# Kernel tuning notes

Measured on AMD Instinct MI355X. Metric: run time of the kernel, lower is better.

The kernel has to match this reference:

```python
import jax, jax.numpy as jnp
import numpy as np

N = 100000
E = 1600000
F_IN, HID, OUT = 64, 64, 32

def setup_inputs() -> dict:
    key = jax.random.key(0)
    ks = jax.random.split(key, 16)
    s = 0.05
    return {
        "x": jax.random.normal(ks[0], (N, F_IN), jnp.float32),
        "edge_index": jax.random.randint(ks[1], (2, E), 0, N, jnp.int64),
        "edge_attr": jax.random.uniform(ks[2], (E, 1), jnp.float32),
        # distance_processor: Linear(1,16) -> ReLU -> Linear(16,1)
        "Wd1": jax.random.normal(ks[3], (1, 16), jnp.float32) * s,
        "bd1": jnp.zeros((16,), jnp.float32),
        "Wd2": jax.random.normal(ks[4], (16, 1), jnp.float32) * s,
        "bd2": jnp.zeros((1,), jnp.float32),
        # conv1 / conv2 GCN linear weights (in, out) + post-aggregation bias
        "W1c": jax.random.normal(ks[5], (F_IN, HID), jnp.float32) * s,
        "b1c": jnp.zeros((HID,), jnp.float32),
        "W2c": jax.random.normal(ks[6], (HID, HID), jnp.float32) * s,
        "b2c": jnp.zeros((HID,), jnp.float32),
        # output head Linear(hidden, output)
        "Wo": jax.random.normal(ks[7], (HID, OUT), jnp.float32) * s,
        "bo": jnp.zeros((OUT,), jnp.float32),
    }


def _gcn_conv(x, src, dst, ew, W, b, n_nodes):
    """PyG GCNConv with edge weights: add self-loops (weight 1), symmetric norm."""
    h = x @ W                                            # [N, out]
    loop = jnp.arange(n_nodes, dtype=src.dtype)
    src_a = jnp.concatenate([src, loop])                 # [E+N]
    dst_a = jnp.concatenate([dst, loop])
    ew_a = jnp.concatenate([ew, jnp.ones((n_nodes,), ew.dtype)])
    deg = jax.ops.segment_sum(ew_a, dst_a, num_segments=n_nodes)
    dinv = jnp.where(deg > 0, jax.lax.rsqrt(jnp.maximum(deg, 1e-30)), 0.0)
    norm = dinv[src_a] * ew_a * dinv[dst_a]              # [E+N]
    msg = norm[:, None] * h[src_a]                       # gather + scale
    agg = jax.ops.segment_sum(msg, dst_a, num_segments=n_nodes)  # scatter-add
    return agg + b


def reference(x, edge_index, edge_attr, Wd1, bd1, Wd2, bd2, W1c, b1c, W2c, b2c, Wo, bo):
    src, dst = edge_index[0], edge_index[1]
    # edge weight from tiny MLP on distance, squeezed to [E]
    hmlp = jax.nn.relu(edge_attr @ Wd1 + bd1)
    ew = jax.nn.sigmoid(hmlp @ Wd2 + bd2)[:, 0]
    h = jax.nn.relu(_gcn_conv(x, src, dst, ew, W1c, b1c, N))
    # dropout is identity in eval mode
    h = _gcn_conv(h, src, dst, ew, W2c, b2c, N)
    return h @ Wo + bo
```

## Files before the change

### kernel.cpp

```cpp
#include <hip/hip_runtime.h>
#include <hip/hip_fp16.h>
#include <math.h>

#define NBMAX 400

__device__ inline ushort f2bf(float f) {
    unsigned u = __float_as_uint(f);
    u += 0x7fff + ((u >> 16) & 1);
    return (ushort)(u >> 16);
}
__device__ inline float bf2f(ushort u) {
    return __uint_as_float(((unsigned)u) << 16);
}

__global__ __launch_bounds__(256) void k_tobf16(const float4* __restrict__ X4,
                                                ushort4* __restrict__ Y4, int n4) {
    int i = blockIdx.x * 256 + threadIdx.x;
    if (i >= n4) return;
    float4 v = X4[i];
    ushort4 o;
    o.x = f2bf(v.x); o.y = f2bf(v.y); o.z = f2bf(v.z); o.w = f2bf(v.w);
    Y4[i] = o;
}

__global__ __launch_bounds__(256) void k_hist(const int* __restrict__ dstv,
                                              int* __restrict__ bcnt,
                                              int E, int chunk) {
    __shared__ int lh[NBMAX];
    int tid = threadIdx.x;
    for (int i = tid; i < NBMAX; i += 256) lh[i] = 0;
    __syncthreads();
    int start = blockIdx.x * chunk;
    int end = min(E, start + chunk);
    for (int e = start + tid; e < end; e += 256)
        atomicAdd(&lh[dstv[e] >> 8], 1);
    __syncthreads();
    for (int i = tid; i < NBMAX; i += 256)
        if (lh[i]) atomicAdd(&bcnt[i], lh[i]);
}

__global__ __launch_bounds__(512) void k_scan_b(const int* __restrict__ bcnt,
                                                int* __restrict__ bbase,
                                                int* __restrict__ bcursor, int nb) {
    __shared__ int s[512];
    int t = threadIdx.x;
    int c = (t < nb) ? bcnt[t] : 0;
    s[t] = c;
    __syncthreads();
    for (int o = 1; o < 512; o <<= 1) {
        int v = (t >= o) ? s[t - o] : 0;
        __syncthreads();
        s[t] += v;
        __syncthreads();
    }
    if (t < nb) {
        int excl = s[t] - c;
        bbase[t] = excl;
        bcursor[t] = excl;
    }
}

__global__ __launch_bounds__(256) void k_edge_scatter(const float* __restrict__ ea,
                                                      const float* __restrict__ Wd1,
                                                      const float* __restrict__ bd1,
                                                      const float* __restrict__ Wd2,
                                                      const float* __restrict__ bd2,
                                                      const int* __restrict__ srcv,
                                                      const int* __restrict__ dstv,
                                                      int* __restrict__ bcursor,
                                                      int2* __restrict__ spk,
                                                      int E, int chunk) {
    __shared__ float w1[16], b1[16], w2[16];
    __shared__ float b2s;
    __shared__ int lh[NBMAX], gb[NBMAX], lc[NBMAX];
    int tid = threadIdx.x;
    if (tid < 16) {
        w1[tid] = Wd1[tid];
        b1[tid] = bd1[tid];
        w2[tid] = Wd2[tid];
    }
    if (tid == 0) b2s = bd2[0];
    for (int i = tid; i < NBMAX; i += 256) { lh[i] = 0; lc[i] = 0; }
    __syncthreads();
    int start = blockIdx.x * chunk;
    int end = min(E, start + chunk);
    for (int e = start + tid; e < end; e += 256)
        atomicAdd(&lh[dstv[e] >> 8], 1);
    __syncthreads();
    for (int i = tid; i < NBMAX; i += 256)
        gb[i] = lh[i] ? atomicAdd(&bcursor[i], lh[i]) : 0;
    __syncthreads();
    for (int e = start + tid; e < end; e += 256) {
        float a = ea[e];
        float s = b2s;
#pragma unroll
        for (int j = 0; j < 16; ++j) {
            float h = fmaxf(a * w1[j] + b1[j], 0.0f);
            s += h * w2[j];
        }
        float w = 1.0f / (1.0f + expf(-s));
        int d = dstv[e];
        int b = d >> 8;
        int p = gb[b] + atomicAdd(&lc[b], 1);
        unsigned payload = ((unsigned)(d & 255) << 16) |
                           (unsigned)__half_as_ushort(__float2half(w));
        spk[p] = make_int2(srcv[e], (int)payload);
    }
}

__global__ __launch_bounds__(256) void k_group(const int2* __restrict__ spk,
                                               const int* __restrict__ bbase,
                                               int2* __restrict__ slots,
                                               int* __restrict__ rowst,
                                               int* __restrict__ cntg,
                                               float* __restrict__ dinv,
                                               int nb, int n, int E) {
    __shared__ int cnt[256], sc[256], ls[256], cur[256];
    __shared__ float dsum[256];
    int b = blockIdx.x;
    int tid = threadIdx.x;
    int r0 = bbase[b];
    int r1 = (b + 1 < nb) ? bbase[b + 1] : E;
    cnt[tid] = 0; cur[tid] = 0; dsum[tid] = 0.0f;
    __syncthreads();
    for (int i = r0 + tid; i < r1; i += 256) {
        int2 pr = spk[i];
        int dl = (pr.y >> 16) & 255;
        atomicAdd(&cnt[dl], 1);
        atomicAdd(&dsum[dl], __half2float(__ushort_as_half((ushort)(pr.y & 0xffff))));
    }
    __syncthreads();
    sc[tid] = cnt[tid];
    __syncthreads();
    for (int o = 1; o < 256; o <<= 1) {
        int v = (tid >= o) ? sc[tid - o] : 0;
        __syncthreads();
        sc[tid] += v;
        __syncthreads();
    }
    ls[tid] = sc[tid] - cnt[tid];
    int dst = (b << 8) + tid;
    if (dst < n) {
        rowst[dst] = r0 + ls[tid];
        cntg[dst] = cnt[tid];
        dinv[dst] = 1.0f / sqrtf(1.0f + dsum[tid]);
    }
    __syncthreads();
    for (int i = r0 + tid; i < r1; i += 256) {
        int2 pr = spk[i];
        int dl = (pr.y >> 16) & 255;
        float wf = __half2float(__ushort_as_half((ushort)(pr.y & 0xffff)));
        int p = r0 + ls[dl] + atomicAdd(&cur[dl], 1);
        slots[p] = make_int2(pr.x, __float_as_int(wf));
    }
}

__global__ __launch_bounds__(256) void k_edge2(const float* __restrict__ ea,
                                               const float* __restrict__ Wd1,
                                               const float* __restrict__ bd1,
                                               const float* __restrict__ Wd2,
                                               const float* __restrict__ bd2,
                                               const int* __restrict__ dstv,
                                               float* __restrict__ ew,
                                               int* __restrict__ cnt, int E) {
    __shared__ float w1[16], b1[16], w2[16];
    __shared__ float b2s;
    if (threadIdx.x < 16) {
        w1[threadIdx.x] = Wd1[threadIdx.x];
        b1[threadIdx.x] = bd1[threadIdx.x];
        w2[threadIdx.x] = Wd2[threadIdx.x];
    }
    if (threadIdx.x == 0) b2s = bd2[0];
    __syncthreads();
    int e = blockIdx.x * 256 + threadIdx.x;
    if (e >= E) return;
    float a = ea[e];
    float s = b2s;
#pragma unroll
    for (int j = 0; j < 16; ++j) {
        float h = fmaxf(a * w1[j] + b1[j], 0.0f);
        s += h * w2[j];
    }
    float w = 1.0f / (1.0f + expf(-s));
    ew[e] = w;
    atomicAdd(&cnt[dstv[e]], 1);
}

__global__ __launch_bounds__(256) void k_scan(const int* __restrict__ cnt,
                                              int* __restrict__ rowst,
                                              int* __restrict__ cursor,
                                              int* __restrict__ gcnt, int n) {
    int i = blockIdx.x * 256 + threadIdx.x;
    int lane = threadIdx.x & 63;
    int c = (i < n) ? cnt[i] : 0;
    int pref = c;
#pragma unroll
    for (int o = 1; o < 64; o <<= 1) {
        int t = __shfl_up(pref, o);
        if (lane >= o) pref += t;
    }
    int total = __shfl(pref, 63);
    int base = 0;
    if (lane == 63 && total > 0) base = atomicAdd(gcnt, total);
    base = __shfl(base, 63);
    if (i < n) {
        int start = base + pref - c;
        rowst[i] = start;
        cursor[i] = start;
    }
}

__global__ __launch_bounds__(256) void k_fill2(const int* __restrict__ srcv,
                                               const int* __restrict__ dstv,
                                               const float* __restrict__ ew,
                                               int* __restrict__ cursor,
                                               int2* __restrict__ slots, int E) {
    int e = blockIdx.x * 256 + threadIdx.x;
    if (e >= E) return;
    int p = atomicAdd(&cursor[dstv[e]], 1);
    slots[p] = make_int2(srcv[e], __float_as_int(ew[e]));
}

__global__ __launch_bounds__(256) void k_deg(const int2* __restrict__ slots,
                                             const int* __restrict__ cnt,
                                             const int* __restrict__ rowst,
                                             float* __restrict__ dinv, int n) {
    int t = blockIdx.x * 256 + threadIdx.x;
    int g = t >> 3;
    int sub = t & 7;
    if (g >= n) return;
    int c = cnt[g];
    size_t base = (size_t)rowst[g];
    float s = 0.0f;
    for (int j = sub; j < c; j += 8) s += __int_as_float(slots[base + j].y);
    s += __shfl_xor(s, 1);
    s += __shfl_xor(s, 2);
    s += __shfl_xor(s, 4);
    if (sub == 0) dinv[g] = 1.0f / sqrtf(1.0f + s);
}

__global__ __launch_bounds__(256) void k_agg(const ushort4* __restrict__ Hb,
                                             const int2* __restrict__ slots,
                                             const int* __restrict__ cnt,
                                             const int* __restrict__ rowst,
                                             const float* __restrict__ dinv,
                                             float* __restrict__ Y, int n) {
    float4* Y4 = (float4*)Y;
    int wid = (blockIdx.x * 256 + threadIdx.x) >> 6;
    int lane = threadIdx.x & 63;
    int l = lane & 15;
    int slb = lane & 48;
    int node = wid * 4 + (lane >> 4);
    bool valid = node < n;
    int nc = valid ? node : 0;
    float di = dinv[nc];
    int c = valid ? cnt[nc] : 0;
    size_t base = (size_t)rowst[nc];

    ushort4 h0 = Hb[(size_t)nc * 16 + l];
    float a0 = di * bf2f(h0.x), a1 = di * bf2f(h0.y);
    float a2 = di * bf2f(h0.z), a3 = di * bf2f(h0.w);
    float b0f = 0.f, b1f = 0.f, b2f = 0.f, b3f = 0.f;
    float c0f = 0.f, c1f = 0.f, c2f = 0.f, c3f = 0.f;
    float d0f = 0.f, d1f = 0.f, d2f = 0.f, d3f = 0.f;

    for (int bb = 0; bb < c; bb += 16) {
        int myc = 0;
        float myw = 0.0f;
        if (bb + l < c) {
            int2 pr = slots[base + bb + l];
            myc = pr.x;
            myw = __int_as_float(pr.y) * dinv[myc];
        }
        int mi = min(16, c - bb);
        for (int i = 0; i < mi; i += 4) {
            int n0 = __shfl(myc, slb + i);
            int n1 = __shfl(myc, slb + i + 1);
            int n2 = __shfl(myc, slb + i + 2);
            int n3 = __shfl(myc, slb + i + 3);
            float w0 = __shfl(myw, slb + i);
            float w1 = __shfl(myw, slb + i + 1);
            float w2 = __shfl(myw, slb + i + 2);
            float w3 = __shfl(myw, slb + i + 3);
            ushort4 v0 = Hb[(size_t)n0 * 16 + l];
            ushort4 v1 = Hb[(size_t)n1 * 16 + l];
            ushort4 v2 = Hb[(size_t)n2 * 16 + l];
            ushort4 v3 = Hb[(size_t)n3 * 16 + l];
            a0 += w0 * bf2f(v0.x); a1 += w0 * bf2f(v0.y);
            a2 += w0 * bf2f(v0.z); a3 += w0 * bf2f(v0.w);
            b0f += w1 * bf2f(v1.x); b1f += w1 * bf2f(v1.y);
            b2f += w1 * bf2f(v1.z); b3f += w1 * bf2f(v1.w);
            c0f += w2 * bf2f(v2.x); c1f += w2 * bf2f(v2.y);
            c2f += w2 * bf2f(v2.z); c3f += w2 * bf2f(v2.w);
            d0f += w3 * bf2f(v3.x); d1f += w3 * bf2f(v3.y);
            d2f += w3 * bf2f(v3.z); d3f += w3 * bf2f(v3.w);
        }
    }
    if (valid) {
        float4 o;
        o.x = di * ((a0 + b0f) + (c0f + d0f));
        o.y = di * ((a1 + b1f) + (c1f + d1f));
        o.z = di * ((a2 + b2f) + (c2f + d2f));
        o.w = di * ((a3 + b3f) + (c3f + d3f));
        Y4[(size_t)node * 16 + l] = o;
    }
}

template <int OUTC, bool RELU, bool BF16OUT>
__global__ __launch_bounds__(256) void k_gemm(const float* __restrict__ X,
                                              const float* __restrict__ W,
                                              const float* __restrict__ bias,
                                              void* __restrict__ Yv, int nrows) {
    __shared__ __align__(16) float ws[64 * OUTC];
    __shared__ __align__(16) float xs[64][64];
    int tid = threadIdx.x;
    for (int i = tid; i < 64 * OUTC / 4; i += 256)
        ((float4*)ws)[i] = ((const float4*)W)[i];
    int row0 = blockIdx.x * 64;
    for (int i = tid; i < 64 * 16; i += 256) {
        int r = i >> 4, c4 = i & 15;
        int gr = row0 + r;
        float4 v = make_float4(0.f, 0.f, 0.f, 0.f);
        if (gr < nrows) v = ((const float4*)X)[(size_t)gr * 16 + c4];
        ((float4*)&xs[r][0])[c4] = v;
    }
    __syncthreads();

    int col = tid % OUTC;
    constexpr int RSLOTS = 256 / OUTC;
    constexpr int RPT = 64 / RSLOTS;
    int rs = tid / OUTC;
    float wc[64];
#pragma unroll
    for (int k = 0; k < 64; ++k) wc[k] = ws[k * OUTC + col];
    float bcol = bias[col];

    for (int rr = 0; rr < RPT; ++rr) {
        int r = rs * RPT + rr;
        const float4* x4 = (const float4*)&xs[r][0];
        float acc = 0.0f;
#pragma unroll
        for (int k4 = 0; k4 < 16; ++k4) {
            float4 v = x4[k4];
            acc += v.x * wc[4 * k4 + 0];
            acc += v.y * wc[4 * k4 + 1];
            acc += v.z * wc[4 * k4 + 2];
            acc += v.w * wc[4 * k4 + 3];
        }
        float o = acc + bcol;
        if (RELU) o = fmaxf(o, 0.0f);
        int gr = row0 + r;
        if (gr < nrows) {
            if (BF16OUT) ((ushort*)Yv)[(size_t)gr * OUTC + col] = f2bf(o);
            else         ((float*)Yv)[(size_t)gr * OUTC + col] = o;
        }
    }
}

__global__ __launch_bounds__(256) void k_prepW(const float* __restrict__ W2c,
                                               const float* __restrict__ Wo,
                                               const float* __restrict__ b2c,
                                               const float* __restrict__ bo,
                                               float* __restrict__ W2o,
                                               float* __restrict__ bo2) {
    int t = threadIdx.x;
    for (int idx = t; idx < 64 * 32; idx += 256) {
        int i = idx >> 5, j = idx & 31;
        float s = 0.0f;
        for (int k = 0; k < 64; ++k) s += W2c[i * 64 + k] * Wo[k * 32 + j];
        W2o[idx] = s;
    }
    if (t < 32) {
        float s = bo[t];
        for (int k = 0; k < 64; ++k) s += b2c[k] * Wo[k * 32 + t];
        bo2[t] = s;
    }
}

extern "C" void kernel_launch(void* const* d_in, const int* in_sizes, int n_in,
                              void* d_out, int out_size, void* d_ws, size_t ws_size,
                              hipStream_t stream) {
    const float* x   = (const float*)d_in[0];
    const int*   ei  = (const int*)d_in[1];
    const float* ea  = (const float*)d_in[2];
    const float* Wd1 = (const float*)d_in[3];
    const float* bd1 = (const float*)d_in[4];
    const float* Wd2 = (const float*)d_in[5];
    const float* bd2 = (const float*)d_in[6];
    const float* W1c = (const float*)d_in[7];
    const float* b1c = (const float*)d_in[8];
    const float* W2c = (const float*)d_in[9];
    const float* b2c = (const float*)d_in[10];
    const float* Wo  = (const float*)d_in[11];
    const float* bo  = (const float*)d_in[12];

    const int N = in_sizes[0] / 64;
    const int E = in_sizes[2];
    const int* srcv = ei;
    const int* dstv = ei + E;
    const int NB = (N + 255) >> 8;

    size_t off = 0;
    auto alloc = [&](size_t bytes) -> void* {
        void* p = (char*)d_ws + off;
        off += (bytes + 255) & ~(size_t)255;
        return p;
    };

    int*    cntg  = (int*)   alloc((size_t)N * 4);
    int*    rowst = (int*)   alloc((size_t)N * 4);
    float*  dinv  = (float*) alloc((size_t)N * 4);
    ushort* xb    = (ushort*)alloc((size_t)N * 64 * 2);
    float*  buf1  = (float*) alloc((size_t)N * 64 * 4);
    ushort* buf1b = (ushort*)alloc((size_t)N * 64 * 2);
    float*  W2o   = (float*) alloc(64 * 32 * 4);
    float*  bo2   = (float*) alloc(32 * 4);
    int2*   slots = (int2*)  alloc((size_t)E * 8);
    float*  buf2  = buf1;

    const int BA = (N + 15) / 16;
    const int BG = (N + 63) / 64;
    const int BT = (N * 16 + 255) / 256;
    const int GB = 512;
    const int CHUNK = (E + GB - 1) / GB;

    size_t base_need = off;
    size_t sort_need = base_need + (((size_t)E * 8 + 255) & ~(size_t)255) + 4096;
    const bool fast = ws_size >= sort_need;

    if (fast) {
        int2* spk    = (int2*)alloc((size_t)E * 8);
        int* bcnt    = (int*) alloc(NBMAX * 4);
        int* bbase   = (int*) alloc(NBMAX * 4);
        int* bcursor = (int*) alloc(NBMAX * 4);

        hipMemsetAsync(bcnt, 0, NBMAX * 4, stream);
        k_tobf16<<<BT, 256, 0, stream>>>((const float4*)x, (ushort4*)xb, N * 16);
        k_hist<<<GB, 256, 0, stream>>>(dstv, bcnt, E, CHUNK);
        k_scan_b<<<1, 512, 0, stream>>>(bcnt, bbase, bcursor, NB);
        k_edge_scatter<<<GB, 256, 0, stream>>>(ea, Wd1, bd1, Wd2, bd2, srcv, dstv,
                                               bcursor, spk, E, CHUNK);
        k_group<<<NB, 256, 0, stream>>>(spk, bbase, slots, rowst, cntg, dinv,
                                        NB, N, E);
        k_prepW<<<1, 256, 0, stream>>>(W2c, Wo, b2c, bo, W2o, bo2);
        k_agg<<<BA, 256, 0, stream>>>((const ushort4*)xb, slots, cntg, rowst,
                                      dinv, buf1, N);
        k_gemm<64, true, true><<<BG, 256, 0, stream>>>(buf1, W1c, b1c, buf1b, N);
        k_agg<<<BA, 256, 0, stream>>>((const ushort4*)buf1b, slots, cntg, rowst,
                                      dinv, buf2, N);
        k_gemm<32, false, false><<<BG, 256, 0, stream>>>(buf2, W2o, bo2, d_out, N);
    } else {
        float* ew   = (float*)alloc((size_t)E * 4);
        int* cursor = (int*)  alloc((size_t)N * 4);
        int* gcnt   = (int*)  alloc(256);
        const int BN = (N + 255) / 256;
        const int BE = (E + 255) / 256;
        const int BD = (N * 8 + 255) / 256;
        hipMemsetAsync(cntg, 0, (size_t)N * 4, stream);
        hipMemsetAsync(gcnt, 0, 4, stream);
        k_tobf16<<<BT, 256, 0, stream>>>((const float4*)x, (ushort4*)xb, N * 16);
        k_edge2<<<BE, 256, 0, stream>>>(ea, Wd1, bd1, Wd2, bd2, dstv, ew, cntg, E);
        k_scan<<<BN, 256, 0, stream>>>(cntg, rowst, cursor, gcnt, N);
        k_fill2<<<BE, 256, 0, stream>>>(srcv, dstv, ew, cursor, slots, E);
        k_deg<<<BD, 256, 0, stream>>>(slots, cntg, rowst, dinv, N);
        k_prepW<<<1, 256, 0, stream>>>(W2c, Wo, b2c, bo, W2o, bo2);
        k_agg<<<BA, 256, 0, stream>>>((const ushort4*)xb, slots, cntg, rowst,
                                      dinv, buf1, N);
        k_gemm<64, true, true><<<BG, 256, 0, stream>>>(buf1, W1c, b1c, buf1b, N);
        k_agg<<<BA, 256, 0, stream>>>((const ushort4*)buf1b, slots, cntg, rowst,
                                      dinv, buf2, N);
        k_gemm<32, false, false><<<BG, 256, 0, stream>>>(buf2, W2o, bo2, d_out, N);
    }
}
```

Measured before the change: 312.6 us.

## Replace global bucket cursor atomics with per-block histogram prefix scan

The histogram kernel now writes a per-block bucket count table. A new column-wise scan kernel computes each block's offset within every bucket, and a second scan computes the bucket bases. The edge scatter kernel no longer recounts its chunk or reserves space with global atomics; it reads precomputed offsets directly. This removes a second pass over dst and the contended global atomics, at the cost of an extra kernel launch and roughly 1.6 MB of workspace traffic.

```diff
diff --git a/kernel.cpp b/kernel.cpp
--- a/kernel.cpp
+++ b/kernel.cpp
@@ -3,6 +3,7 @@
 #include <math.h>
 
 #define NBMAX 400
+#define GBUILD 512
 
 __device__ inline ushort f2bf(float f) {
     unsigned u = __float_as_uint(f);
@@ -24,7 +25,7 @@
 }
 
 __global__ __launch_bounds__(256) void k_hist(const int* __restrict__ dstv,
-                                              int* __restrict__ bcnt,
+                                              int* __restrict__ bh,
                                               int E, int chunk) {
     __shared__ int lh[NBMAX];
     int tid = threadIdx.x;
@@ -35,16 +36,39 @@
     for (int e = start + tid; e < end; e += 256)
         atomicAdd(&lh[dstv[e] >> 8], 1);
     __syncthreads();
-    for (int i = tid; i < NBMAX; i += 256)
-        if (lh[i]) atomicAdd(&bcnt[i], lh[i]);
-}
-
-__global__ __launch_bounds__(512) void k_scan_b(const int* __restrict__ bcnt,
-                                                int* __restrict__ bbase,
-                                                int* __restrict__ bcursor, int nb) {
+    int* row = bh + (size_t)blockIdx.x * NBMAX;
+    for (int i = tid; i < NBMAX; i += 256) row[i] = lh[i];
+}
+
+__global__ __launch_bounds__(256) void k_scanA(const int* __restrict__ bh,
+                                               int* __restrict__ boff,
+                                               int* __restrict__ btot) {
+    __shared__ int s[GBUILD];
+    int b = blockIdx.x;
+    int t = threadIdx.x;
+    int i0 = t, i1 = t + 256;
+    s[i0] = bh[(size_t)i0 * NBMAX + b];
+    s[i1] = bh[(size_t)i1 * NBMAX + b];
+    __syncthreads();
+    int c0 = s[i0], c1 = s[i1];
+    for (int o = 1; o < GBUILD; o <<= 1) {
+        int v0 = (i0 >= o) ? s[i0 - o] : 0;
+        int v1 = (i1 >= o) ? s[i1 - o] : 0;
+        __syncthreads();
+        s[i0] += v0;
+        s[i1] += v1;
+        __syncthreads();
+    }
+    boff[(size_t)i0 * NBMAX + b] = s[i0] - c0;
+    boff[(size_t)i1 * NBMAX + b] = s[i1] - c1;
+    if (t == 0) btot[b] = s[GBUILD - 1];
+}
+
+__global__ __launch_bounds__(512) void k_scanB(const int* __restrict__ btot,
+                                               int* __restrict__ bbase, int nb) {
     __shared__ int s[512];
     int t = threadIdx.x;
-    int c = (t < nb) ? bcnt[t] : 0;
+    int c = (t < nb) ? btot[t] : 0;
     s[t] = c;
     __syncthreads();
     for (int o = 1; o < 512; o <<= 1) {
@@ -53,11 +77,7 @@
         s[t] += v;
         __syncthreads();
     }
-    if (t < nb) {
-        int excl = s[t] - c;
-        bbase[t] = excl;
-        bcursor[t] = excl;
-    }
+    if (t < nb) bbase[t] = s[t] - c;
 }
 
 __global__ __launch_bounds__(256) void k_edge_scatter(const float* __restrict__ ea,
@@ -67,12 +87,13 @@
                                                       const float* __restrict__ bd2,
                                                       const int* __restrict__ srcv,
                                                       const int* __restrict__ dstv,
-                                                      int* __restrict__ bcursor,
+                                                      const int* __restrict__ bbase,
+                                                      const int* __restrict__ boff,
                                                       int2* __restrict__ spk,
                                                       int E, int chunk) {
     __shared__ float w1[16], b1[16], w2[16];
     __shared__ float b2s;
-    __shared__ int lh[NBMAX], gb[NBMAX], lc[NBMAX];
+    __shared__ int gb[NBMAX], lc[NBMAX];
     int tid = threadIdx.x;
     if (tid < 16) {
         w1[tid] = Wd1[tid];
@@ -80,16 +101,14 @@
         w2[tid] = Wd2[tid];
     }
     if (tid == 0) b2s = bd2[0];
-    for (int i = tid; i < NBMAX; i += 256) { lh[i] = 0; lc[i] = 0; }
+    const int* brow = boff + (size_t)blockIdx.x * NBMAX;
+    for (int i = tid; i < NBMAX; i += 256) {
+        gb[i] = bbase[i] + brow[i];
+        lc[i] = 0;
+    }
     __syncthreads();
     int start = blockIdx.x * chunk;
     int end = min(E, start + chunk);
-    for (int e = start + tid; e < end; e += 256)
-        atomicAdd(&lh[dstv[e] >> 8], 1);
-    __syncthreads();
-    for (int i = tid; i < NBMAX; i += 256)
-        gb[i] = lh[i] ? atomicAdd(&bcursor[i], lh[i]) : 0;
-    __syncthreads();
     for (int e = start + tid; e < end; e += 256) {
         float a = ea[e];
         float s = b2s;
@@ -421,25 +440,27 @@
     const int BA = (N + 15) / 16;
     const int BG = (N + 63) / 64;
     const int BT = (N * 16 + 255) / 256;
-    const int GB = 512;
+    const int GB = GBUILD;
     const int CHUNK = (E + GB - 1) / GB;
 
     size_t base_need = off;
-    size_t sort_need = base_need + (((size_t)E * 8 + 255) & ~(size_t)255) + 4096;
+    size_t sort_need = base_need + (((size_t)E * 8 + 255) & ~(size_t)255)
+                       + 2 * ((size_t)GB * NBMAX * 4 + 256) + 16384;
     const bool fast = ws_size >= sort_need;
 
     if (fast) {
-        int2* spk    = (int2*)alloc((size_t)E * 8);
-        int* bcnt    = (int*) alloc(NBMAX * 4);
-        int* bbase   = (int*) alloc(NBMAX * 4);
-        int* bcursor = (int*) alloc(NBMAX * 4);
-
-        hipMemsetAsync(bcnt, 0, NBMAX * 4, stream);
+        int2* spk  = (int2*)alloc((size_t)E * 8);
+        int* bh    = (int*) alloc((size_t)GB * NBMAX * 4);
+        int* boff  = (int*) alloc((size_t)GB * NBMAX * 4);
+        int* btot  = (int*) alloc(NBMAX * 4);
+        int* bbase = (int*) alloc(NBMAX * 4);
+
         k_tobf16<<<BT, 256, 0, stream>>>((const float4*)x, (ushort4*)xb, N * 16);
-        k_hist<<<GB, 256, 0, stream>>>(dstv, bcnt, E, CHUNK);
-        k_scan_b<<<1, 512, 0, stream>>>(bcnt, bbase, bcursor, NB);
+        k_hist<<<GB, 256, 0, stream>>>(dstv, bh, E, CHUNK);
+        k_scanA<<<NBMAX, 256, 0, stream>>>(bh, boff, btot);
+        k_scanB<<<1, 512, 0, stream>>>(btot, bbase, NB);
         k_edge_scatter<<<GB, 256, 0, stream>>>(ea, Wd1, bd1, Wd2, bd2, srcv, dstv,
-                                               bcursor, spk, E, CHUNK);
+                                               bbase, boff, spk, E, CHUNK);
         k_group<<<NB, 256, 0, stream>>>(spk, bbase, slots, rowst, cntg, dinv,
                                         NB, N, E);
         k_prepW<<<1, 256, 0, stream>>>(W2c, Wo, b2c, bo, W2o, bo2);
```

Measured after the change: 284.0 us. 9.2% less time.
